# Performance work log

Hardware: AMD Instinct MI355X
Metric: run time of the kernel (lower is better)

## Reference

```python
import jax, jax.numpy as jnp
import numpy as np

D_MODEL = 2048
NUM_HEADS = 16
D_K = D_MODEL // NUM_HEADS
ROPE_THETA = 10000.0
B, S = 2, 2048


def setup_inputs() -> dict:
    key = jax.random.key(0)
    ks = jax.random.split(key, 5)
    std = 1.0 / np.sqrt(D_MODEL)
    return {
        "x": jax.random.normal(ks[0], (B, S, D_MODEL), jnp.float32),
        "wq": jax.random.normal(ks[1], (D_MODEL, D_MODEL), jnp.float32) * std,
        "wk": jax.random.normal(ks[2], (D_MODEL, D_MODEL), jnp.float32) * std,
        "wv": jax.random.normal(ks[3], (D_MODEL, D_MODEL), jnp.float32) * std,
        "wo": jax.random.normal(ks[4], (D_MODEL, D_MODEL), jnp.float32) * std,
        "token_positions": jnp.arange(S, dtype=jnp.int32),
    }


def _rope(x, positions):
    # x: [b, h, s, d_k]; positions: [s]
    inv_freq = 1.0 / (ROPE_THETA ** (jnp.arange(0, D_K, 2, dtype=jnp.float32) / D_K))
    freqs = positions.astype(jnp.float32)[:, None] * inv_freq[None, :]  # [s, d_k/2]
    cos, sin = jnp.cos(freqs), jnp.sin(freqs)
    x_even, x_odd = x[..., ::2], x[..., 1::2]
    out_even = x_even * cos - x_odd * sin
    out_odd = x_even * sin + x_odd * cos
    # re-interleave even/odd lanes
    return jnp.stack([out_even, out_odd], axis=-1).reshape(x.shape)


def reference(x, wq, wk, wv, wo, token_positions):
    b, s, _ = x.shape
    # projections: weight is [out, in] as in torch Linear-style einsum
    q = jnp.einsum("bsd,ed->bse", x, wq)
    k = jnp.einsum("bsd,ed->bse", x, wk)
    v = jnp.einsum("bsd,ed->bse", x, wv)
    # split heads: b s (h d) -> b h s d
    def split(t):
        return t.reshape(b, s, NUM_HEADS, D_K).transpose(0, 2, 1, 3)
    q, k, v = split(q), split(k), split(v)
    q = _rope(q, token_positions)
    k = _rope(k, token_positions)
    scores = jnp.einsum("bhmd,bhnd->bhmn", q, k) / jnp.sqrt(jnp.float32(D_K))
    causal = jnp.tril(jnp.ones((s, s), dtype=bool))
    scores = jnp.where(causal[None, None], scores, -jnp.inf)
    attn = jax.nn.softmax(scores, axis=-1)
    out = jnp.einsum("bhmn,bhnd->bhmd", attn, v)
    out = out.transpose(0, 2, 1, 3).reshape(b, s, D_MODEL)
    return jnp.einsum("em,bsm->bse", wo, out)
```

## Files before the change

### kernel.cpp

```cpp
#include <hip/hip_runtime.h>

#define S_LEN 2048
#define DM 2048
#define NH 16
#define DK 128
#define BB 2
#define BH (BB*NH)
#define GK 2048

typedef float f32x4 __attribute__((ext_vector_type(4)));
typedef float f32x16 __attribute__((ext_vector_type(16)));
typedef __bf16 bf16x8 __attribute__((ext_vector_type(8)));
typedef __bf16 bf16x2 __attribute__((ext_vector_type(2)));
typedef unsigned int u32;

#define AS1 __attribute__((address_space(1)))
#define AS3 __attribute__((address_space(3)))

__device__ inline void gload16(const void* g, void* l){
  __builtin_amdgcn_global_load_lds((AS1 const u32*)g, (AS3 u32*)l, 16, 0, 0);
}

__device__ inline ushort f2bf(float f){
  __bf16 h = (__bf16)f;
  ushort u;
  __builtin_memcpy(&u, &h, 2);
  return u;
}

__device__ inline u32 cvtpk(float a, float b){
  bf16x2 p; p[0] = (__bf16)a; p[1] = (__bf16)b;
  u32 r; __builtin_memcpy(&r, &p, 4); return r;
}

__global__ void k_f32_to_bf16(const float* __restrict__ in, ushort* __restrict__ out, int n4){
  int i = blockIdx.x * blockDim.x + threadIdx.x;
  if (i >= n4) return;
  float4 v = reinterpret_cast<const float4*>(in)[i];
  ushort4 o;
  o.x = f2bf(v.x); o.y = f2bf(v.y); o.z = f2bf(v.z); o.w = f2bf(v.w);
  reinterpret_cast<ushort4*>(out)[i] = o;
}

__global__ void k_w4(const float* __restrict__ wq, const float* __restrict__ wk,
                     const float* __restrict__ wv, const float* __restrict__ wo4,
                     ushort* __restrict__ dqkv, ushort* __restrict__ dwo){
  int i = blockIdx.x * 256 + threadIdx.x;
  int sel = i >> 20;
  int off = i & ((1 << 20) - 1);
  const float* s = (sel == 0) ? wq : (sel == 1) ? wk : (sel == 2) ? wv : wo4;
  ushort* d = (sel < 3) ? (dqkv + (size_t)sel * DM * DM) : dwo;
  float4 v = reinterpret_cast<const float4*>(s)[off];
  ushort4 o;
  o.x = f2bf(v.x); o.y = f2bf(v.y); o.z = f2bf(v.z); o.w = f2bf(v.w);
  reinterpret_cast<ushort4*>(d)[off] = o;
}

__global__ void k_rope_table(const int* __restrict__ pos, float2* __restrict__ cs){
  int idx = blockIdx.x * 256 + threadIdx.x;
  if (idx >= S_LEN * 64) return;
  int s = idx >> 6, i = idx & 63;
  float inv = expf(-0.14391156831212787f * (float)i);
  float f = (float)pos[s] * inv;
  cs[idx] = make_float2(cosf(f), sinf(f));
}

#define SBAR() do{ __builtin_amdgcn_s_barrier(); __builtin_amdgcn_sched_barrier(0); }while(0)
#define VMC(n) asm volatile("s_waitcnt vmcnt(" #n ")" ::: "memory")

#define STG(slot, srcp, tks, khh) do{ \
  const ushort* _s = (srcp) + (tks)*64 + (khh)*32; \
  gload16(_s,                    lds + (slot)*8192 + wid*512); \
  gload16(_s + (size_t)128*GK,   lds + (slot)*8192 + 4096 + wid*512); \
}while(0)

#define RD_A(slot, mh) do{ \
  af[0] = *reinterpret_cast<const bf16x8*>(ldsc + (slot)*16384 + wm*8192 + ((mh)*4+0)*1024 + frA); \
  af[1] = *reinterpret_cast<const bf16x8*>(ldsc + (slot)*16384 + wm*8192 + ((mh)*4+1)*1024 + frA); \
  af[2] = *reinterpret_cast<const bf16x8*>(ldsc + (slot)*16384 + wm*8192 + ((mh)*4+2)*1024 + frA); \
  af[3] = *reinterpret_cast<const bf16x8*>(ldsc + (slot)*16384 + wm*8192 + ((mh)*4+3)*1024 + frA); \
}while(0)

#define RD_B(slot) do{ \
  bfr[0] = *reinterpret_cast<const bf16x8*>(ldsc + (slot)*16384 + wn*4096 + 0*1024 + frA); \
  bfr[1] = *reinterpret_cast<const bf16x8*>(ldsc + (slot)*16384 + wn*4096 + 1*1024 + frA); \
  bfr[2] = *reinterpret_cast<const bf16x8*>(ldsc + (slot)*16384 + wn*4096 + 2*1024 + frA); \
  bfr[3] = *reinterpret_cast<const bf16x8*>(ldsc + (slot)*16384 + wn*4096 + 3*1024 + frA); \
}while(0)

#define MM(mh) do{ \
  __builtin_amdgcn_s_setprio(1); \
  _Pragma("unroll") \
  for (int mf2 = 0; mf2 < 4; mf2++) \
    _Pragma("unroll") \
    for (int nf = 0; nf < 4; nf++) \
      acc[(mh)*4+mf2][nf] = __builtin_amdgcn_mfma_f32_16x16x32_bf16(af[mf2], bfr[nf], acc[(mh)*4+mf2][nf], 0, 0, 0); \
  __builtin_amdgcn_s_setprio(0); \
}while(0)

__launch_bounds__(512, 2)
__global__ void k_gemm_qk(const ushort* __restrict__ A, const ushort* __restrict__ Bt,
                          const float2* __restrict__ cs,
                          ushort* __restrict__ Qh, ushort* __restrict__ Kh){
  __shared__ short lds[65536];
  const int tid = threadIdx.x, lane = tid & 63, wid = tid >> 6;
  const int wm = wid >> 2, wn = wid & 3;
  const int fr = lane & 15, fq = lane >> 4;

  const int bid = blockIdx.x;
  const int b2 = (bid & 7) * 32 + (bid >> 3);
  const int by = b2 >> 4, bx = b2 & 15;

  const int rbase = wid * 16 + (lane >> 2);
  const int kup = ((lane & 3) ^ ((lane >> 3) & 3)) * 8;
  const ushort* pa = A  + (size_t)(by * 256 + rbase) * GK + kup;
  const ushort* pb = Bt + (size_t)(bx * 256 + rbase) * GK + kup;

  const char* ldsc = (const char*)lds;
  const int frA = fr * 64 + ((fq * 16) ^ (((fr >> 1) & 3) << 4));

  f32x4 acc[8][4] = {};
  bf16x8 af[4], bfr[4];

  STG(0, pa, 0, 0); STG(1, pb, 0, 0); STG(2, pa, 0, 1); STG(3, pb, 0, 1);
  STG(4, pa, 1, 0); STG(5, pb, 1, 0);
  VMC(8);
  SBAR();

  #pragma unroll 1
  for (int it = 0; it < 16; ++it){
    const int tb  = 2 * it + 1;
    const int tn  = (2 * it + 2 < 32) ? 2 * it + 2 : 31;
    const int tn1 = (2 * it + 3 < 32) ? 2 * it + 3 : 31;
    RD_A(0, 0); RD_B(1); STG(6, pa, tb, 1);           SBAR(); MM(0); SBAR();
    RD_A(0, 1);          STG(7, pb, tb, 1);  VMC(6);  SBAR(); MM(1); SBAR();
    RD_A(2, 0); RD_B(3); STG(0, pa, tn, 0);           SBAR(); MM(0); SBAR();
    RD_A(2, 1);          STG(1, pb, tn, 0);  VMC(6);  SBAR(); MM(1); SBAR();
    RD_A(4, 0); RD_B(5); STG(2, pa, tn, 1);           SBAR(); MM(0); SBAR();
    RD_A(4, 1);          STG(3, pb, tn, 1);  VMC(6);  SBAR(); MM(1); SBAR();
    RD_A(6, 0); RD_B(7); STG(4, pa, tn1, 0);          SBAR(); MM(0); SBAR();
    RD_A(6, 1);          STG(5, pb, tn1, 0); VMC(6);  SBAR(); MM(1); SBAR();
  }

  const int rowb = by * 256 + wm * 128 + fq * 4;
  const bool isQ = (bx < 8);
  ushort* dst = isQ ? Qh : Kh;
  const float qscl = isQ ? 0.08838834764831845f : 1.0f;
  #pragma unroll
  for (int mf = 0; mf < 8; mf++)
    #pragma unroll
    for (int nf = 0; nf < 4; nf++){
      int col = bx * 256 + wn * 64 + nf * 16 + fr;
      int cg = col & 2047;
      int hh = cg >> 7, dd = cg & 127, jj = (cg >> 1) & 63;
      #pragma unroll
      for (int i = 0; i < 4; i++){
        int row = rowb + mf * 16 + i;
        int s = row & (S_LEN - 1), bb = row >> 11;
        float2 c2 = cs[s * 64 + jj];
        float v = acc[mf][nf][i];
        float p = __shfl_xor(v, 1);
        float o = (fr & 1) ? fmaf(p, c2.y, v * c2.x) : fmaf(v, c2.x, -p * c2.y);
        dst[((size_t)(bb * NH + hh) * S_LEN + s) * DK + dd] = f2bf(o * qscl);
      }
    }
}

#define WSTG_A(si, tks, khh) do{ \
  const ushort* _s = pa + (tks)*64 + (khh)*32; \
  gload16(_s,                  lds + (si)*8192 + wid*512); \
  gload16(_s + (size_t)128*GK, lds + (si)*8192 + 4096 + wid*512); \
}while(0)
#define WSTG_B(si, tks, khh) do{ \
  const ushort* _s = pb + (tks)*64 + (khh)*32; \
  gload16(_s, lds + 32768 + (si)*4096 + wid*512); \
}while(0)
#define WRD_A(si, mhf) do{ \
  af[0] = *reinterpret_cast<const bf16x8*>(ldsc + (si)*16384 + wm*4096 + ((mhf)*2+0)*1024 + frA); \
  af[1] = *reinterpret_cast<const bf16x8*>(ldsc + (si)*16384 + wm*4096 + ((mhf)*2+1)*1024 + frA); \
}while(0)
#define WRD_B(si) do{ \
  bfr[0] = *reinterpret_cast<const bf16x8*>(ldsc + 65536 + (si)*8192 + wn*4096 + 0*1024 + frA); \
  bfr[1] = *reinterpret_cast<const bf16x8*>(ldsc + 65536 + (si)*8192 + wn*4096 + 1*1024 + frA); \
  bfr[2] = *reinterpret_cast<const bf16x8*>(ldsc + 65536 + (si)*8192 + wn*4096 + 2*1024 + frA); \
  bfr[3] = *reinterpret_cast<const bf16x8*>(ldsc + 65536 + (si)*8192 + wn*4096 + 3*1024 + frA); \
}while(0)
#define WMM(mhf) do{ \
  __builtin_amdgcn_s_setprio(1); \
  _Pragma("unroll") \
  for (int k2 = 0; k2 < 2; k2++) \
    _Pragma("unroll") \
    for (int nf = 0; nf < 4; nf++) \
      acc[(mhf)*2+k2][nf] = __builtin_amdgcn_mfma_f32_16x16x32_bf16(af[k2], bfr[nf], acc[(mhf)*2+k2][nf], 0, 0, 0); \
  __builtin_amdgcn_s_setprio(0); \
}while(0)

#define WBODY() \
  WSTG_A(0, 0, 0); WSTG_B(0, 0, 0); WSTG_A(1, 0, 1); WSTG_B(1, 0, 1); \
  WSTG_A(2, 1, 0); WSTG_B(2, 1, 0); \
  VMC(6); \
  SBAR(); \
  _Pragma("unroll 1") \
  for (int it = 0; it < 16; ++it){ \
    const int tb  = 2 * it + 1; \
    const int tn  = (2 * it + 2 < 32) ? 2 * it + 2 : 31; \
    const int tn1 = (2 * it + 3 < 32) ? 2 * it + 3 : 31; \
    WRD_A(0, 0); WRD_B(0); WSTG_A(3, tb, 1);            SBAR(); WMM(0); SBAR(); \
    WRD_A(0, 1);           WSTG_B(3, tb, 1);  VMC(6);   SBAR(); WMM(1); SBAR(); \
    WRD_A(1, 0); WRD_B(1); WSTG_A(0, tn, 0);            SBAR(); WMM(0); SBAR(); \
    WRD_A(1, 1);           WSTG_B(0, tn, 0);  VMC(6);   SBAR(); WMM(1); SBAR(); \
    WRD_A(2, 0); WRD_B(2); WSTG_A(1, tn, 1);            SBAR(); WMM(0); SBAR(); \
    WRD_A(2, 1);           WSTG_B(1, tn, 1);  VMC(6);   SBAR(); WMM(1); SBAR(); \
    WRD_A(3, 0); WRD_B(3); WSTG_A(2, tn1, 0);           SBAR(); WMM(0); SBAR(); \
    WRD_A(3, 1);           WSTG_B(2, tn1, 0); VMC(6);   SBAR(); WMM(1); SBAR(); \
  }

__launch_bounds__(512, 2)
__global__ void k_gemm_v(const ushort* __restrict__ A, const ushort* __restrict__ Bt,
                         ushort* __restrict__ Vt){
  __shared__ short lds[49152];
  const int tid = threadIdx.x, lane = tid & 63, wid = tid >> 6;
  const int wm = wid >> 1, wn = wid & 1;
  const int fr = lane & 15, fq = lane >> 4;

  const int bid = blockIdx.x;
  const int b2 = (bid & 7) * 32 + (bid >> 3);
  const int by = b2 >> 4, bx = b2 & 15;

  const int rbase = wid * 16 + (lane >> 2);
  const int kup = ((lane & 3) ^ ((lane >> 3) & 3)) * 8;
  const ushort* pa = A  + (size_t)(by * 256 + rbase) * GK + kup;
  const ushort* pb = Bt + (size_t)(bx * 128 + rbase) * GK + kup;

  const char* ldsc = (const char*)lds;
  const int frA = fr * 64 + ((fq * 16) ^ (((fr >> 1) & 3) << 4));

  f32x4 acc[4][4] = {};
  bf16x8 af[2], bfr[4];

  WBODY();

  const int rowb = by * 256 + wm * 64 + fq * 4;
  #pragma unroll
  for (int mf = 0; mf < 4; mf++){
    int row0 = rowb + mf * 16;
    int s0 = row0 & (S_LEN - 1), bb = row0 >> 11;
    #pragma unroll
    for (int nf = 0; nf < 4; nf++){
      int col = bx * 128 + wn * 64 + nf * 16 + fr;
      int hh = col >> 7, dd = col & 127;
      ushort4 o;
      o.x = f2bf(acc[mf][nf][0]); o.y = f2bf(acc[mf][nf][1]);
      o.z = f2bf(acc[mf][nf][2]); o.w = f2bf(acc[mf][nf][3]);
      *reinterpret_cast<ushort4*>(&Vt[((size_t)(bb * NH + hh) * DK + dd) * S_LEN + s0]) = o;
    }
  }
}

__launch_bounds__(512, 2)
__global__ void k_gemm_wo(const ushort* __restrict__ A, const ushort* __restrict__ Bt,
                          float* __restrict__ C){
  __shared__ short lds[49152];
  const int tid = threadIdx.x, lane = tid & 63, wid = tid >> 6;
  const int wm = wid >> 1, wn = wid & 1;
  const int fr = lane & 15, fq = lane >> 4;

  const int bid = blockIdx.x;
  const int b2 = (bid & 7) * 32 + (bid >> 3);
  const int by = b2 >> 4, bx = b2 & 15;

  const int rbase = wid * 16 + (lane >> 2);
  const int kup = ((lane & 3) ^ ((lane >> 3) & 3)) * 8;
  const ushort* pa = A  + (size_t)(by * 256 + rbase) * GK + kup;
  const ushort* pb = Bt + (size_t)(bx * 128 + rbase) * GK + kup;

  const char* ldsc = (const char*)lds;
  const int frA = fr * 64 + ((fq * 16) ^ (((fr >> 1) & 3) << 4));

  f32x4 acc[4][4] = {};
  bf16x8 af[2], bfr[4];

  WBODY();

  const int orow = by * 256 + wm * 64 + fq * 4;
  const int ocol = bx * 128 + wn * 64 + fr;
  #pragma unroll
  for (int mf = 0; mf < 4; mf++)
    #pragma unroll
    for (int nf = 0; nf < 4; nf++)
      #pragma unroll
      for (int i = 0; i < 4; i++)
        C[(size_t)(orow + mf * 16 + i) * DM + ocol + nf * 16] = acc[mf][nf][i];
}

__launch_bounds__(256, 2)
__global__ void k_attn(const ushort* __restrict__ Q, const ushort* __restrict__ K,
                       const ushort* __restrict__ Vt, ushort* __restrict__ O){
  __shared__ short Kt[2][64 * 128];
  __shared__ short Vl[2][128 * 64];
  const int tid = threadIdx.x, lane = tid & 63, wid = tid >> 6;
  const int bid = blockIdx.x;
  const int bh = bid & 31, b = bh >> 4, hh = bh & 15;
  const int t8 = (bid >> 5) & 7;
  const int j = (bid < 256) ? (15 - t8) : t8;
  const int nt = 2 * j + 2;
  const int ql = lane & 31, h = lane >> 5;
  const int qrb = j * 128 + wid * 32;
  const int qrow = qrb + ql;
  const int swz = (ql & 7) << 4;

  const ushort* kbp = K  + (size_t)bh * S_LEN * DK;
  const ushort* vbp = Vt + (size_t)bh * DK * S_LEN;
  ushort* ob = O + (size_t)b * S_LEN * DM;

  int kro[4], kco[4], vro[4], vco[4];
  #pragma unroll
  for (int jj = 0; jj < 4; jj++){
    int ins = wid * 4 + jj;
    kro[jj] = ins * 4 + (lane >> 4);
    kco[jj] = 8 * ((lane & 15) ^ (kro[jj] & 7));
    vro[jj] = ins * 8 + (lane >> 3);
    vco[jj] = 8 * ((lane & 7) ^ (vro[jj] & 7));
  }

  bf16x8 qf[8];
  #pragma unroll
  for (int s = 0; s < 8; s++)
    qf[s] = *reinterpret_cast<const bf16x8*>(
        Q + ((size_t)bh * S_LEN + qrow) * DK + s * 16 + h * 8);

  float mi = -1e30f, li = 0.f;
  f32x16 accO[4] = {};

  #pragma unroll
  for (int jj = 0; jj < 4; jj++){
    int ins = wid * 4 + jj;
    gload16(kbp + (size_t)kro[jj] * DK + kco[jj],      (char*)Kt + ins * 1024);
    gload16(vbp + (size_t)vro[jj] * S_LEN + vco[jj],   (char*)Vl + ins * 1024);
  }
  __syncthreads();

  #pragma unroll 1
  for (int kt = 0; kt < nt; kt++){
    const int k0 = kt * 64;
    const int cur = kt & 1;
    if (kt + 1 < nt){
      const int k1 = k0 + 64;
      #pragma unroll
      for (int jj = 0; jj < 4; jj++){
        int ins = wid * 4 + jj;
        gload16(kbp + (size_t)(k1 + kro[jj]) * DK + kco[jj],  (char*)Kt + (cur ^ 1) * 16384 + ins * 1024);
        gload16(vbp + (size_t)vro[jj] * S_LEN + k1 + vco[jj], (char*)Vl + (cur ^ 1) * 16384 + ins * 1024);
      }
    }
    const char* KtB = (const char*)Kt + cur * 16384;
    const char* VlB = (const char*)Vl + cur * 16384;

    f32x16 sc[2] = {};
    #pragma unroll
    for (int s = 0; s < 8; s++){
      bf16x8 kf0 = *reinterpret_cast<const bf16x8*>(
          KtB + (ql) * 256 + ((s * 32 + h * 16) ^ swz));
      bf16x8 kf1 = *reinterpret_cast<const bf16x8*>(
          KtB + (32 + ql) * 256 + ((s * 32 + h * 16) ^ swz));
      sc[0] = __builtin_amdgcn_mfma_f32_32x32x16_bf16(kf0, qf[s], sc[0], 0, 0, 0);
      sc[1] = __builtin_amdgcn_mfma_f32_32x32x16_bf16(kf1, qf[s], sc[1], 0, 0, 0);
    }

    if (k0 + 63 > qrb){
      #pragma unroll
      for (int kb = 0; kb < 2; kb++)
        #pragma unroll
        for (int r = 0; r < 16; r++)
          if (k0 + kb * 32 + (r & 3) + 8 * (r >> 2) + 4 * h > qrow) sc[kb][r] = -1e30f;
    }

    float mx = sc[0][0];
    #pragma unroll
    for (int kb = 0; kb < 2; kb++)
      #pragma unroll
      for (int r = 0; r < 16; r++) mx = fmaxf(mx, sc[kb][r]);
    mx = fmaxf(mx, __shfl_xor(mx, 32));

    if (!__all(mx <= mi + 8.0f)){
      float mn = fmaxf(mi, mx);
      float scl = __expf(mi - mn);
      mi = mn;
      li *= scl;
      float sclr[16];
      #pragma unroll
      for (int r = 0; r < 16; r++) sclr[r] = __shfl(scl, (r & 3) + 8 * (r >> 2) + 4 * h);
      #pragma unroll
      for (int dt = 0; dt < 4; dt++)
        #pragma unroll
        for (int r = 0; r < 16; r++) accO[dt][r] *= sclr[r];
    }

    float rs = 0.f;
    #pragma unroll
    for (int kb = 0; kb < 2; kb++)
      #pragma unroll
      for (int r = 0; r < 16; r++){
        float e = __expf(sc[kb][r] - mi);
        sc[kb][r] = e;
        rs += e;
      }
    rs += __shfl_xor(rs, 32);
    li += rs;

    bf16x8 pf[4];
    #pragma unroll
    for (int t = 0; t < 4; t++){
      const int kbb = t >> 1, rb = (t & 1) * 8;
      u32 wA0 = cvtpk(sc[kbb][rb + 0], sc[kbb][rb + 1]);
      u32 wA1 = cvtpk(sc[kbb][rb + 2], sc[kbb][rb + 3]);
      u32 wB0 = cvtpk(sc[kbb][rb + 4], sc[kbb][rb + 5]);
      u32 wB1 = cvtpk(sc[kbb][rb + 6], sc[kbb][rb + 7]);
      u32 X = h ? wA0 : wB0;
      u32 Y = h ? wA1 : wB1;
      u32 x0 = (u32)__shfl_xor((int)X, 32);
      u32 x1 = (u32)__shfl_xor((int)Y, 32);
      u32 f[4];
      f[0] = h ? x0 : wA0;
      f[1] = h ? x1 : wA1;
      f[2] = h ? wB0 : x0;
      f[3] = h ? wB1 : x1;
      __builtin_memcpy(&pf[t], f, 16);
    }

    #pragma unroll
    for (int dt = 0; dt < 4; dt++){
      const int vrow = dt * 32 + ql;
      const int vswz = (vrow & 7) << 4;
      #pragma unroll
      for (int t = 0; t < 4; t++){
        bf16x8 vf = *reinterpret_cast<const bf16x8*>(
            VlB + vrow * 128 + ((t * 32 + h * 16) ^ vswz));
        accO[dt] = __builtin_amdgcn_mfma_f32_32x32x16_bf16(pf[t], vf, accO[dt], 0, 0, 0);
      }
    }
    __syncthreads();
  }

  float invr[16];
  #pragma unroll
  for (int r = 0; r < 16; r++) invr[r] = 1.f / __shfl(li, (r & 3) + 8 * (r >> 2) + 4 * h);
  #pragma unroll
  for (int dt = 0; dt < 4; dt++)
    #pragma unroll
    for (int r = 0; r < 16; r++){
      int row = qrb + (r & 3) + 8 * (r >> 2) + 4 * h;
      ob[(size_t)row * DM + hh * DK + dt * 32 + ql] = f2bf(accO[dt][r] * invr[r]);
    }
}

extern "C" void kernel_launch(void* const* d_in, const int* in_sizes, int n_in,
                              void* d_out, int out_size, void* d_ws, size_t ws_size,
                              hipStream_t stream){
  const float* x  = (const float*)d_in[0];
  const float* wq = (const float*)d_in[1];
  const float* wk = (const float*)d_in[2];
  const float* wv = (const float*)d_in[3];
  const float* wo = (const float*)d_in[4];
  const int* pos  = (const int*)d_in[5];
  float* out = (float*)d_out;

  char* ws = (char*)d_ws;
  ushort* xb   = (ushort*)(ws);
  ushort* Ob   = xb;
  ushort* wqkv = (ushort*)(ws + 16777216);
  ushort* Qh   = (ushort*)(ws + 41943040);
  ushort* Kh   = (ushort*)(ws + 58720256);
  ushort* Vt   = (ushort*)(ws + 75497472);
  float2* cs   = (float2*)(ws + 92274688);
  ushort* wob  = (ushort*)(ws + 93323264);

  const int M = BB * S_LEN;

  k_rope_table<<<(S_LEN * 64) / 256, 256, 0, stream>>>(pos, cs);
  k_f32_to_bf16<<<(M * DM / 4) / 256, 256, 0, stream>>>(x, xb, M * DM / 4);
  k_w4<<<4 * (DM * DM / 4) / 256, 256, 0, stream>>>(wq, wk, wv, wo, wqkv, wob);

  k_gemm_qk<<<256, 512, 0, stream>>>(xb, wqkv, cs, Qh, Kh);
  k_gemm_v<<<256, 512, 0, stream>>>(xb, wqkv + (size_t)2 * DM * DM, Vt);

  k_attn<<<512, 256, 0, stream>>>(Qh, Kh, Vt, Ob);

  k_gemm_wo<<<256, 512, 0, stream>>>(Ob, wob, out);
}
```

Before: 247.8 us.

## Software-pipeline attention QK with softmax/PV and merge conversion kernels

The attention main loop is restructured so each wave computes the QK^T scores for the next key tile while it does softmax and PV for the current tile. Two score register sets alternate, and the K and V loads are issued at separate points around the barriers. The goal is to overlap MFMA work with the exp/shuffle softmax work and with global-to-LDS loads. Separately, the x and weight fp32-to-bf16 conversion kernels are merged into one launch to save launch overhead. The extra score registers raise register pressure under the two-blocks-per-CU launch bound.

```diff
diff --git a/kernel.cpp b/kernel.cpp
--- a/kernel.cpp
+++ b/kernel.cpp
@@ -33,23 +33,20 @@
   u32 r; __builtin_memcpy(&r, &p, 4); return r;
 }
 
-__global__ void k_f32_to_bf16(const float* __restrict__ in, ushort* __restrict__ out, int n4){
-  int i = blockIdx.x * blockDim.x + threadIdx.x;
-  if (i >= n4) return;
-  float4 v = reinterpret_cast<const float4*>(in)[i];
-  ushort4 o;
-  o.x = f2bf(v.x); o.y = f2bf(v.y); o.z = f2bf(v.z); o.w = f2bf(v.w);
-  reinterpret_cast<ushort4*>(out)[i] = o;
-}
-
-__global__ void k_w4(const float* __restrict__ wq, const float* __restrict__ wk,
-                     const float* __restrict__ wv, const float* __restrict__ wo4,
-                     ushort* __restrict__ dqkv, ushort* __restrict__ dwo){
+__global__ void k_conv(const float* __restrict__ x, const float* __restrict__ wq,
+                       const float* __restrict__ wk, const float* __restrict__ wv,
+                       const float* __restrict__ wo4,
+                       ushort* __restrict__ xb, ushort* __restrict__ dqkv,
+                       ushort* __restrict__ dwo){
   int i = blockIdx.x * 256 + threadIdx.x;
   int sel = i >> 20;
   int off = i & ((1 << 20) - 1);
-  const float* s = (sel == 0) ? wq : (sel == 1) ? wk : (sel == 2) ? wv : wo4;
-  ushort* d = (sel < 3) ? (dqkv + (size_t)sel * DM * DM) : dwo;
+  const float* s; ushort* d;
+  if (sel < 2){ s = x + ((size_t)sel << 22); d = xb + ((size_t)sel << 22); }
+  else if (sel == 2){ s = wq; d = dqkv; }
+  else if (sel == 3){ s = wk; d = dqkv + (size_t)DM * DM; }
+  else if (sel == 4){ s = wv; d = dqkv + (size_t)2 * DM * DM; }
+  else { s = wo4; d = dwo; }
   float4 v = reinterpret_cast<const float4*>(s)[off];
   ushort4 o;
   o.x = f2bf(v.x); o.y = f2bf(v.y); o.z = f2bf(v.z); o.w = f2bf(v.w);
@@ -293,6 +290,78 @@
         C[(size_t)(orow + mf * 16 + i) * DM + ocol + nf * 16] = acc[mf][nf][i];
 }
 
+#define STK(tt) do{ char* _kd = (char*)Kt + ((tt) & 1) * 16384; \
+  _Pragma("unroll") for (int jj = 0; jj < 4; jj++){ \
+    int ins = wid * 4 + jj; \
+    gload16(kbp + (size_t)((tt) * 64 + kro[jj]) * DK + kco[jj], _kd + ins * 1024); } }while(0)
+
+#define STV(tt) do{ char* _vd = (char*)Vl + ((tt) & 1) * 16384; \
+  _Pragma("unroll") for (int jj = 0; jj < 4; jj++){ \
+    int ins = wid * 4 + jj; \
+    gload16(vbp + (size_t)vro[jj] * S_LEN + (tt) * 64 + vco[jj], _vd + ins * 1024); } }while(0)
+
+#define QKS(SC, tt) do{ \
+  const char* _KtB = (const char*)Kt + ((tt) & 1) * 16384; \
+  f32x16 _z = {}; SC[0] = _z; SC[1] = _z; \
+  _Pragma("unroll") for (int s = 0; s < 8; s++){ \
+    bf16x8 kf0 = *reinterpret_cast<const bf16x8*>(_KtB + ql * 256 + ((s*32 + h*16) ^ swz)); \
+    bf16x8 kf1 = *reinterpret_cast<const bf16x8*>(_KtB + (32 + ql) * 256 + ((s*32 + h*16) ^ swz)); \
+    SC[0] = __builtin_amdgcn_mfma_f32_32x32x16_bf16(kf0, qf[s], SC[0], 0, 0, 0); \
+    SC[1] = __builtin_amdgcn_mfma_f32_32x32x16_bf16(kf1, qf[s], SC[1], 0, 0, 0); \
+  } }while(0)
+
+#define SMPV(SC, tt) do{ \
+  const int _k0 = (tt) * 64; \
+  const char* _VlB = (const char*)Vl + ((tt) & 1) * 16384; \
+  if (_k0 + 63 > qrb){ \
+    _Pragma("unroll") for (int kb = 0; kb < 2; kb++) \
+      _Pragma("unroll") for (int r = 0; r < 16; r++) \
+        if (_k0 + kb * 32 + (r & 3) + 8 * (r >> 2) + 4 * h > qrow) SC[kb][r] = -1e30f; \
+  } \
+  float mx = SC[0][0]; \
+  _Pragma("unroll") for (int kb = 0; kb < 2; kb++) \
+    _Pragma("unroll") for (int r = 0; r < 16; r++) mx = fmaxf(mx, SC[kb][r]); \
+  mx = fmaxf(mx, __shfl_xor(mx, 32)); \
+  if (!__all(mx <= mi + 8.0f)){ \
+    float mn = fmaxf(mi, mx); \
+    float scl = __expf(mi - mn); \
+    mi = mn; li *= scl; \
+    float sclr[16]; \
+    _Pragma("unroll") for (int r = 0; r < 16; r++) sclr[r] = __shfl(scl, (r & 3) + 8 * (r >> 2) + 4 * h); \
+    _Pragma("unroll") for (int dt = 0; dt < 4; dt++) \
+      _Pragma("unroll") for (int r = 0; r < 16; r++) accO[dt][r] *= sclr[r]; \
+  } \
+  float rs = 0.f; \
+  _Pragma("unroll") for (int kb = 0; kb < 2; kb++) \
+    _Pragma("unroll") for (int r = 0; r < 16; r++){ \
+      float e = __expf(SC[kb][r] - mi); SC[kb][r] = e; rs += e; } \
+  rs += __shfl_xor(rs, 32); \
+  li += rs; \
+  bf16x8 pf[4]; \
+  _Pragma("unroll") for (int t2 = 0; t2 < 4; t2++){ \
+    const int kbb = t2 >> 1, rb = (t2 & 1) * 8; \
+    u32 wA0 = cvtpk(SC[kbb][rb + 0], SC[kbb][rb + 1]); \
+    u32 wA1 = cvtpk(SC[kbb][rb + 2], SC[kbb][rb + 3]); \
+    u32 wB0 = cvtpk(SC[kbb][rb + 4], SC[kbb][rb + 5]); \
+    u32 wB1 = cvtpk(SC[kbb][rb + 6], SC[kbb][rb + 7]); \
+    u32 X = h ? wA0 : wB0; \
+    u32 Y = h ? wA1 : wB1; \
+    u32 x0 = (u32)__shfl_xor((int)X, 32); \
+    u32 x1 = (u32)__shfl_xor((int)Y, 32); \
+    u32 fw[4]; \
+    fw[0] = h ? x0 : wA0; fw[1] = h ? x1 : wA1; \
+    fw[2] = h ? wB0 : x0; fw[3] = h ? wB1 : x1; \
+    __builtin_memcpy(&pf[t2], fw, 16); \
+  } \
+  _Pragma("unroll") for (int dt = 0; dt < 4; dt++){ \
+    const int vrow = dt * 32 + ql; \
+    const int vswz = (vrow & 7) << 4; \
+    _Pragma("unroll") for (int t2 = 0; t2 < 4; t2++){ \
+      bf16x8 vf = *reinterpret_cast<const bf16x8*>(_VlB + vrow * 128 + ((t2 * 32 + h * 16) ^ vswz)); \
+      accO[dt] = __builtin_amdgcn_mfma_f32_32x32x16_bf16(pf[t2], vf, accO[dt], 0, 0, 0); \
+    } \
+  } }while(0)
+
 __launch_bounds__(256, 2)
 __global__ void k_attn(const ushort* __restrict__ Q, const ushort* __restrict__ K,
                        const ushort* __restrict__ Vt, ushort* __restrict__ O){
@@ -331,116 +400,33 @@
 
   float mi = -1e30f, li = 0.f;
   f32x16 accO[4] = {};
-
-  #pragma unroll
-  for (int jj = 0; jj < 4; jj++){
-    int ins = wid * 4 + jj;
-    gload16(kbp + (size_t)kro[jj] * DK + kco[jj],      (char*)Kt + ins * 1024);
-    gload16(vbp + (size_t)vro[jj] * S_LEN + vco[jj],   (char*)Vl + ins * 1024);
+  f32x16 scA[2], scB[2];
+
+  STK(0); STV(0);
+  __syncthreads();
+  STK(1);
+  QKS(scA, 0);
+  __syncthreads();
+  STV(1);
+
+  int t = 1;
+  #pragma unroll 1
+  for (; t + 1 < nt; t += 2){
+    STK(t + 1);
+    QKS(scB, t);
+    SMPV(scA, t - 1);
+    __syncthreads();
+    STV(t + 1);
+    STK(t + 2);
+    QKS(scA, t + 1);
+    SMPV(scB, t);
+    __syncthreads();
+    STV(t + 2);
   }
+  QKS(scB, t);
+  SMPV(scA, t - 1);
   __syncthreads();
-
-  #pragma unroll 1
-  for (int kt = 0; kt < nt; kt++){
-    const int k0 = kt * 64;
-    const int cur = kt & 1;
-    if (kt + 1 < nt){
-      const int k1 = k0 + 64;
-      #pragma unroll
-      for (int jj = 0; jj < 4; jj++){
-        int ins = wid * 4 + jj;
-        gload16(kbp + (size_t)(k1 + kro[jj]) * DK + kco[jj],  (char*)Kt + (cur ^ 1) * 16384 + ins * 1024);
-        gload16(vbp + (size_t)vro[jj] * S_LEN + k1 + vco[jj], (char*)Vl + (cur ^ 1) * 16384 + ins * 1024);
-      }
-    }
-    const char* KtB = (const char*)Kt + cur * 16384;
-    const char* VlB = (const char*)Vl + cur * 16384;
-
-    f32x16 sc[2] = {};
-    #pragma unroll
-    for (int s = 0; s < 8; s++){
-      bf16x8 kf0 = *reinterpret_cast<const bf16x8*>(
-          KtB + (ql) * 256 + ((s * 32 + h * 16) ^ swz));
-      bf16x8 kf1 = *reinterpret_cast<const bf16x8*>(
-          KtB + (32 + ql) * 256 + ((s * 32 + h * 16) ^ swz));
-      sc[0] = __builtin_amdgcn_mfma_f32_32x32x16_bf16(kf0, qf[s], sc[0], 0, 0, 0);
-      sc[1] = __builtin_amdgcn_mfma_f32_32x32x16_bf16(kf1, qf[s], sc[1], 0, 0, 0);
-    }
-
-    if (k0 + 63 > qrb){
-      #pragma unroll
-      for (int kb = 0; kb < 2; kb++)
-        #pragma unroll
-        for (int r = 0; r < 16; r++)
-          if (k0 + kb * 32 + (r & 3) + 8 * (r >> 2) + 4 * h > qrow) sc[kb][r] = -1e30f;
-    }
-
-    float mx = sc[0][0];
-    #pragma unroll
-    for (int kb = 0; kb < 2; kb++)
-      #pragma unroll
-      for (int r = 0; r < 16; r++) mx = fmaxf(mx, sc[kb][r]);
-    mx = fmaxf(mx, __shfl_xor(mx, 32));
-
-    if (!__all(mx <= mi + 8.0f)){
-      float mn = fmaxf(mi, mx);
-      float scl = __expf(mi - mn);
-      mi = mn;
-      li *= scl;
-      float sclr[16];
-      #pragma unroll
-      for (int r = 0; r < 16; r++) sclr[r] = __shfl(scl, (r & 3) + 8 * (r >> 2) + 4 * h);
-      #pragma unroll
-      for (int dt = 0; dt < 4; dt++)
-        #pragma unroll
-        for (int r = 0; r < 16; r++) accO[dt][r] *= sclr[r];
-    }
-
-    float rs = 0.f;
-    #pragma unroll
-    for (int kb = 0; kb < 2; kb++)
-      #pragma unroll
-      for (int r = 0; r < 16; r++){
-        float e = __expf(sc[kb][r] - mi);
-        sc[kb][r] = e;
-        rs += e;
-      }
-    rs += __shfl_xor(rs, 32);
-    li += rs;
-
-    bf16x8 pf[4];
-    #pragma unroll
-    for (int t = 0; t < 4; t++){
-      const int kbb = t >> 1, rb = (t & 1) * 8;
-      u32 wA0 = cvtpk(sc[kbb][rb + 0], sc[kbb][rb + 1]);
-      u32 wA1 = cvtpk(sc[kbb][rb + 2], sc[kbb][rb + 3]);
-      u32 wB0 = cvtpk(sc[kbb][rb + 4], sc[kbb][rb + 5]);
-      u32 wB1 = cvtpk(sc[kbb][rb + 6], sc[kbb][rb + 7]);
-      u32 X = h ? wA0 : wB0;
-      u32 Y = h ? wA1 : wB1;
-      u32 x0 = (u32)__shfl_xor((int)X, 32);
-      u32 x1 = (u32)__shfl_xor((int)Y, 32);
-      u32 f[4];
-      f[0] = h ? x0 : wA0;
-      f[1] = h ? x1 : wA1;
-      f[2] = h ? wB0 : x0;
-      f[3] = h ? wB1 : x1;
-      __builtin_memcpy(&pf[t], f, 16);
-    }
-
-    #pragma unroll
-    for (int dt = 0; dt < 4; dt++){
-      const int vrow = dt * 32 + ql;
-      const int vswz = (vrow & 7) << 4;
-      #pragma unroll
-      for (int t = 0; t < 4; t++){
-        bf16x8 vf = *reinterpret_cast<const bf16x8*>(
-            VlB + vrow * 128 + ((t * 32 + h * 16) ^ vswz));
-        accO[dt] = __builtin_amdgcn_mfma_f32_32x32x16_bf16(pf[t], vf, accO[dt], 0, 0, 0);
-      }
-    }
-    __syncthreads();
-  }
+  SMPV(scB, t);
 
   float invr[16];
   #pragma unroll
@@ -475,11 +461,8 @@
   float2* cs   = (float2*)(ws + 92274688);
   ushort* wob  = (ushort*)(ws + 93323264);
 
-  const int M = BB * S_LEN;
-
   k_rope_table<<<(S_LEN * 64) / 256, 256, 0, stream>>>(pos, cs);
-  k_f32_to_bf16<<<(M * DM / 4) / 256, 256, 0, stream>>>(x, xb, M * DM / 4);
-  k_w4<<<4 * (DM * DM / 4) / 256, 256, 0, stream>>>(wq, wk, wv, wo, wqkv, wob);
+  k_conv<<<24576, 256, 0, stream>>>(x, wq, wk, wv, wo, xb, wqkv, wob);
 
   k_gemm_qk<<<256, 512, 0, stream>>>(xb, wqkv, cs, Qh, Kh);
   k_gemm_v<<<256, 512, 0, stream>>>(xb, wqkv + (size_t)2 * DM * DM, Vt);
```

Measured after the change: 245.3 us. No clear change (-1.0%).

## Merge conversion kernels and restructure attention into paired causal 64-row tiles

Applied to the files above, without the earlier changes.

Merges the rope-table, activation and weight bf16 conversion launches into one kernel to cut launch overhead. Reworks the attention kernel to 128-thread blocks, each handling two 64-row query tiles (j and 31-j) so causal work is balanced per block. It also drops the K/V double buffer for a single-buffered load with two barriers per tile, which loses load/compute overlap and halves waves per block.

```diff
diff --git a/kernel.cpp b/kernel.cpp
--- a/kernel.cpp
+++ b/kernel.cpp
@@ -33,36 +33,34 @@
   u32 r; __builtin_memcpy(&r, &p, 4); return r;
 }
 
-__global__ void k_f32_to_bf16(const float* __restrict__ in, ushort* __restrict__ out, int n4){
-  int i = blockIdx.x * blockDim.x + threadIdx.x;
-  if (i >= n4) return;
-  float4 v = reinterpret_cast<const float4*>(in)[i];
-  ushort4 o;
-  o.x = f2bf(v.x); o.y = f2bf(v.y); o.z = f2bf(v.z); o.w = f2bf(v.w);
-  reinterpret_cast<ushort4*>(out)[i] = o;
-}
-
-__global__ void k_w4(const float* __restrict__ wq, const float* __restrict__ wk,
-                     const float* __restrict__ wv, const float* __restrict__ wo4,
-                     ushort* __restrict__ dqkv, ushort* __restrict__ dwo){
-  int i = blockIdx.x * 256 + threadIdx.x;
+__global__ void k_conv(const float* __restrict__ x, const float* __restrict__ wq,
+                       const float* __restrict__ wk, const float* __restrict__ wv,
+                       const float* __restrict__ wo4,
+                       ushort* __restrict__ xb, ushort* __restrict__ dqkv,
+                       ushort* __restrict__ dwo,
+                       const int* __restrict__ pos, float2* __restrict__ cs){
+  int bid = blockIdx.x;
+  if (bid >= 24576){
+    int idx = (bid - 24576) * 256 + threadIdx.x;
+    int s = idx >> 6, i = idx & 63;
+    float inv = expf(-0.14391156831212787f * (float)i);
+    float f = (float)pos[s] * inv;
+    cs[idx] = make_float2(cosf(f), sinf(f));
+    return;
+  }
+  int i = bid * 256 + threadIdx.x;
   int sel = i >> 20;
   int off = i & ((1 << 20) - 1);
-  const float* s = (sel == 0) ? wq : (sel == 1) ? wk : (sel == 2) ? wv : wo4;
-  ushort* d = (sel < 3) ? (dqkv + (size_t)sel * DM * DM) : dwo;
+  const float* s; ushort* d;
+  if (sel < 2){ s = x + ((size_t)sel << 22); d = xb + ((size_t)sel << 22); }
+  else if (sel == 2){ s = wq; d = dqkv; }
+  else if (sel == 3){ s = wk; d = dqkv + (size_t)DM * DM; }
+  else if (sel == 4){ s = wv; d = dqkv + (size_t)2 * DM * DM; }
+  else { s = wo4; d = dwo; }
   float4 v = reinterpret_cast<const float4*>(s)[off];
   ushort4 o;
   o.x = f2bf(v.x); o.y = f2bf(v.y); o.z = f2bf(v.z); o.w = f2bf(v.w);
   reinterpret_cast<ushort4*>(d)[off] = o;
-}
-
-__global__ void k_rope_table(const int* __restrict__ pos, float2* __restrict__ cs){
-  int idx = blockIdx.x * 256 + threadIdx.x;
-  if (idx >= S_LEN * 64) return;
-  int s = idx >> 6, i = idx & 63;
-  float inv = expf(-0.14391156831212787f * (float)i);
-  float f = (float)pos[s] * inv;
-  cs[idx] = make_float2(cosf(f), sinf(f));
 }
 
 #define SBAR() do{ __builtin_amdgcn_s_barrier(); __builtin_amdgcn_sched_barrier(0); }while(0)
@@ -293,165 +291,158 @@
         C[(size_t)(orow + mf * 16 + i) * DM + ocol + nf * 16] = acc[mf][nf][i];
 }
 
-__launch_bounds__(256, 2)
+__launch_bounds__(128, 2)
 __global__ void k_attn(const ushort* __restrict__ Q, const ushort* __restrict__ K,
                        const ushort* __restrict__ Vt, ushort* __restrict__ O){
-  __shared__ short Kt[2][64 * 128];
-  __shared__ short Vl[2][128 * 64];
+  __shared__ short Kt[64 * 128];
+  __shared__ short Vl[128 * 64];
   const int tid = threadIdx.x, lane = tid & 63, wid = tid >> 6;
   const int bid = blockIdx.x;
-  const int bh = bid & 31, b = bh >> 4, hh = bh & 15;
-  const int t8 = (bid >> 5) & 7;
-  const int j = (bid < 256) ? (15 - t8) : t8;
-  const int nt = 2 * j + 2;
+  const int pid = bid >> 5;
+  const int bh = bid & 31;
+  const int b = bh >> 4, hh = bh & 15;
   const int ql = lane & 31, h = lane >> 5;
-  const int qrb = j * 128 + wid * 32;
-  const int qrow = qrb + ql;
   const int swz = (ql & 7) << 4;
 
   const ushort* kbp = K  + (size_t)bh * S_LEN * DK;
   const ushort* vbp = Vt + (size_t)bh * DK * S_LEN;
   ushort* ob = O + (size_t)b * S_LEN * DM;
 
-  int kro[4], kco[4], vro[4], vco[4];
+  int kro[8], kco[8], vro[8], vco[8];
   #pragma unroll
-  for (int jj = 0; jj < 4; jj++){
-    int ins = wid * 4 + jj;
+  for (int jj = 0; jj < 8; jj++){
+    int ins = wid * 8 + jj;
     kro[jj] = ins * 4 + (lane >> 4);
     kco[jj] = 8 * ((lane & 15) ^ (kro[jj] & 7));
     vro[jj] = ins * 8 + (lane >> 3);
     vco[jj] = 8 * ((lane & 7) ^ (vro[jj] & 7));
   }
 
-  bf16x8 qf[8];
-  #pragma unroll
-  for (int s = 0; s < 8; s++)
-    qf[s] = *reinterpret_cast<const bf16x8*>(
-        Q + ((size_t)bh * S_LEN + qrow) * DK + s * 16 + h * 8);
-
-  float mi = -1e30f, li = 0.f;
-  f32x16 accO[4] = {};
-
-  #pragma unroll
-  for (int jj = 0; jj < 4; jj++){
-    int ins = wid * 4 + jj;
-    gload16(kbp + (size_t)kro[jj] * DK + kco[jj],      (char*)Kt + ins * 1024);
-    gload16(vbp + (size_t)vro[jj] * S_LEN + vco[jj],   (char*)Vl + ins * 1024);
-  }
-  __syncthreads();
-
   #pragma unroll 1
-  for (int kt = 0; kt < nt; kt++){
-    const int k0 = kt * 64;
-    const int cur = kt & 1;
-    if (kt + 1 < nt){
-      const int k1 = k0 + 64;
-      #pragma unroll
-      for (int jj = 0; jj < 4; jj++){
-        int ins = wid * 4 + jj;
-        gload16(kbp + (size_t)(k1 + kro[jj]) * DK + kco[jj],  (char*)Kt + (cur ^ 1) * 16384 + ins * 1024);
-        gload16(vbp + (size_t)vro[jj] * S_LEN + k1 + vco[jj], (char*)Vl + (cur ^ 1) * 16384 + ins * 1024);
+  for (int half = 0; half < 2; half++){
+    const int j = half ? pid : 31 - pid;
+    const int qrb = j * 64 + wid * 32;
+    const int qrow = qrb + ql;
+    const int nt = j + 1;
+
+    bf16x8 qf[8];
+    #pragma unroll
+    for (int s = 0; s < 8; s++)
+      qf[s] = *reinterpret_cast<const bf16x8*>(
+          Q + ((size_t)bh * S_LEN + qrow) * DK + s * 16 + h * 8);
+
+    float mi = -1e30f, li = 0.f;
+    f32x16 accO[4] = {};
+
+    #pragma unroll 1
+    for (int kt = 0; kt < nt; kt++){
+      const int k0 = kt * 64;
+
+      __syncthreads();
+      #pragma unroll
+      for (int jj = 0; jj < 8; jj++){
+        int ins = wid * 8 + jj;
+        gload16(kbp + (size_t)(k0 + kro[jj]) * DK + kco[jj],  (char*)Kt + ins * 1024);
+        gload16(vbp + (size_t)vro[jj] * S_LEN + k0 + vco[jj], (char*)Vl + ins * 1024);
+      }
+      __syncthreads();
+
+      f32x16 sc[2] = {};
+      #pragma unroll
+      for (int s = 0; s < 8; s++){
+        bf16x8 kf0 = *reinterpret_cast<const bf16x8*>(
+            (const char*)Kt + ql * 256 + ((s * 32 + h * 16) ^ swz));
+        bf16x8 kf1 = *reinterpret_cast<const bf16x8*>(
+            (const char*)Kt + (32 + ql) * 256 + ((s * 32 + h * 16) ^ swz));
+        sc[0] = __builtin_amdgcn_mfma_f32_32x32x16_bf16(kf0, qf[s], sc[0], 0, 0, 0);
+        sc[1] = __builtin_amdgcn_mfma_f32_32x32x16_bf16(kf1, qf[s], sc[1], 0, 0, 0);
+      }
+
+      if (k0 + 63 > qrb){
+        #pragma unroll
+        for (int kb = 0; kb < 2; kb++)
+          #pragma unroll
+          for (int r = 0; r < 16; r++)
+            if (k0 + kb * 32 + (r & 3) + 8 * (r >> 2) + 4 * h > qrow) sc[kb][r] = -1e30f;
+      }
+
+      float mx = sc[0][0];
+      #pragma unroll
+      for (int kb = 0; kb < 2; kb++)
+        #pragma unroll
+        for (int r = 0; r < 16; r++) mx = fmaxf(mx, sc[kb][r]);
+      mx = fmaxf(mx, __shfl_xor(mx, 32));
+
+      if (!__all(mx <= mi + 8.0f)){
+        float mn = fmaxf(mi, mx);
+        float scl = __expf(mi - mn);
+        mi = mn;
+        li *= scl;
+        float sclr[16];
+        #pragma unroll
+        for (int r = 0; r < 16; r++) sclr[r] = __shfl(scl, (r & 3) + 8 * (r >> 2) + 4 * h);
+        #pragma unroll
+        for (int dt = 0; dt < 4; dt++)
+          #pragma unroll
+          for (int r = 0; r < 16; r++) accO[dt][r] *= sclr[r];
+      }
+
+      float rs = 0.f;
+      #pragma unroll
+      for (int kb = 0; kb < 2; kb++)
+        #pragma unroll
+        for (int r = 0; r < 16; r++){
+          float e = __expf(sc[kb][r] - mi);
+          sc[kb][r] = e;
+          rs += e;
+        }
+      rs += __shfl_xor(rs, 32);
+      li += rs;
+
+      bf16x8 pf[4];
+      #pragma unroll
+      for (int t = 0; t < 4; t++){
+        const int kbb = t >> 1, rb = (t & 1) * 8;
+        u32 wA0 = cvtpk(sc[kbb][rb + 0], sc[kbb][rb + 1]);
+        u32 wA1 = cvtpk(sc[kbb][rb + 2], sc[kbb][rb + 3]);
+        u32 wB0 = cvtpk(sc[kbb][rb + 4], sc[kbb][rb + 5]);
+        u32 wB1 = cvtpk(sc[kbb][rb + 6], sc[kbb][rb + 7]);
+        u32 X = h ? wA0 : wB0;
+        u32 Y = h ? wA1 : wB1;
+        u32 x0 = (u32)__shfl_xor((int)X, 32);
+        u32 x1 = (u32)__shfl_xor((int)Y, 32);
+        u32 f[4];
+        f[0] = h ? x0 : wA0;
+        f[1] = h ? x1 : wA1;
+        f[2] = h ? wB0 : x0;
+        f[3] = h ? wB1 : x1;
+        __builtin_memcpy(&pf[t], f, 16);
+      }
+
+      #pragma unroll
+      for (int dt = 0; dt < 4; dt++){
+        const int vrow = dt * 32 + ql;
+        const int vswz = (vrow & 7) << 4;
+        #pragma unroll
+        for (int t = 0; t < 4; t++){
+          bf16x8 vf = *reinterpret_cast<const bf16x8*>(
+              (const char*)Vl + vrow * 128 + ((t * 32 + h * 16) ^ vswz));
+          accO[dt] = __builtin_amdgcn_mfma_f32_32x32x16_bf16(pf[t], vf, accO[dt], 0, 0, 0);
+        }
       }
     }
-    const char* KtB = (const char*)Kt + cur * 16384;
-    const char* VlB = (const char*)Vl + cur * 16384;
-
-    f32x16 sc[2] = {};
-    #pragma unroll
-    for (int s = 0; s < 8; s++){
-      bf16x8 kf0 = *reinterpret_cast<const bf16x8*>(
-          KtB + (ql) * 256 + ((s * 32 + h * 16) ^ swz));
-      bf16x8 kf1 = *reinterpret_cast<const bf16x8*>(
-          KtB + (32 + ql) * 256 + ((s * 32 + h * 16) ^ swz));
-      sc[0] = __builtin_amdgcn_mfma_f32_32x32x16_bf16(kf0, qf[s], sc[0], 0, 0, 0);
-      sc[1] = __builtin_amdgcn_mfma_f32_32x32x16_bf16(kf1, qf[s], sc[1], 0, 0, 0);
-    }
-
-    if (k0 + 63 > qrb){
-      #pragma unroll
-      for (int kb = 0; kb < 2; kb++)
-        #pragma unroll
-        for (int r = 0; r < 16; r++)
-          if (k0 + kb * 32 + (r & 3) + 8 * (r >> 2) + 4 * h > qrow) sc[kb][r] = -1e30f;
-    }
-
-    float mx = sc[0][0];
-    #pragma unroll
-    for (int kb = 0; kb < 2; kb++)
-      #pragma unroll
-      for (int r = 0; r < 16; r++) mx = fmaxf(mx, sc[kb][r]);
-    mx = fmaxf(mx, __shfl_xor(mx, 32));
-
-    if (!__all(mx <= mi + 8.0f)){
-      float mn = fmaxf(mi, mx);
-      float scl = __expf(mi - mn);
-      mi = mn;
-      li *= scl;
-      float sclr[16];
-      #pragma unroll
-      for (int r = 0; r < 16; r++) sclr[r] = __shfl(scl, (r & 3) + 8 * (r >> 2) + 4 * h);
-      #pragma unroll
-      for (int dt = 0; dt < 4; dt++)
-        #pragma unroll
-        for (int r = 0; r < 16; r++) accO[dt][r] *= sclr[r];
-    }
-
-    float rs = 0.f;
-    #pragma unroll
-    for (int kb = 0; kb < 2; kb++)
+
+    float invr[16];
+    #pragma unroll
+    for (int r = 0; r < 16; r++) invr[r] = 1.f / __shfl(li, (r & 3) + 8 * (r >> 2) + 4 * h);
+    #pragma unroll
+    for (int dt = 0; dt < 4; dt++)
       #pragma unroll
       for (int r = 0; r < 16; r++){
-        float e = __expf(sc[kb][r] - mi);
-        sc[kb][r] = e;
-        rs += e;
-      }
-    rs += __shfl_xor(rs, 32);
-    li += rs;
-
-    bf16x8 pf[4];
-    #pragma unroll
-    for (int t = 0; t < 4; t++){
-      const int kbb = t >> 1, rb = (t & 1) * 8;
-      u32 wA0 = cvtpk(sc[kbb][rb + 0], sc[kbb][rb + 1]);
-      u32 wA1 = cvtpk(sc[kbb][rb + 2], sc[kbb][rb + 3]);
-      u32 wB0 = cvtpk(sc[kbb][rb + 4], sc[kbb][rb + 5]);
-      u32 wB1 = cvtpk(sc[kbb][rb + 6], sc[kbb][rb + 7]);
-      u32 X = h ? wA0 : wB0;
-      u32 Y = h ? wA1 : wB1;
-      u32 x0 = (u32)__shfl_xor((int)X, 32);
-      u32 x1 = (u32)__shfl_xor((int)Y, 32);
-      u32 f[4];
-      f[0] = h ? x0 : wA0;
-      f[1] = h ? x1 : wA1;
-      f[2] = h ? wB0 : x0;
-      f[3] = h ? wB1 : x1;
-      __builtin_memcpy(&pf[t], f, 16);
-    }
-
-    #pragma unroll
-    for (int dt = 0; dt < 4; dt++){
-      const int vrow = dt * 32 + ql;
-      const int vswz = (vrow & 7) << 4;
-      #pragma unroll
-      for (int t = 0; t < 4; t++){
-        bf16x8 vf = *reinterpret_cast<const bf16x8*>(
-            VlB + vrow * 128 + ((t * 32 + h * 16) ^ vswz));
-        accO[dt] = __builtin_amdgcn_mfma_f32_32x32x16_bf16(pf[t], vf, accO[dt], 0, 0, 0);
-      }
-    }
-    __syncthreads();
-  }
-
-  float invr[16];
-  #pragma unroll
-  for (int r = 0; r < 16; r++) invr[r] = 1.f / __shfl(li, (r & 3) + 8 * (r >> 2) + 4 * h);
-  #pragma unroll
-  for (int dt = 0; dt < 4; dt++)
-    #pragma unroll
-    for (int r = 0; r < 16; r++){
-      int row = qrb + (r & 3) + 8 * (r >> 2) + 4 * h;
-      ob[(size_t)row * DM + hh * DK + dt * 32 + ql] = f2bf(accO[dt][r] * invr[r]);
-    }
+        int row = qrb + (r & 3) + 8 * (r >> 2) + 4 * h;
+        ob[(size_t)row * DM + hh * DK + dt * 32 + ql] = f2bf(accO[dt][r] * invr[r]);
+      }
+  }
 }
 
 extern "C" void kernel_launch(void* const* d_in, const int* in_sizes, int n_in,
@@ -475,16 +466,12 @@
   float2* cs   = (float2*)(ws + 92274688);
   ushort* wob  = (ushort*)(ws + 93323264);
 
-  const int M = BB * S_LEN;
-
-  k_rope_table<<<(S_LEN * 64) / 256, 256, 0, stream>>>(pos, cs);
-  k_f32_to_bf16<<<(M * DM / 4) / 256, 256, 0, stream>>>(x, xb, M * DM / 4);
-  k_w4<<<4 * (DM * DM / 4) / 256, 256, 0, stream>>>(wq, wk, wv, wo, wqkv, wob);
+  k_conv<<<24576 + 512, 256, 0, stream>>>(x, wq, wk, wv, wo, xb, wqkv, wob, pos, cs);
 
   k_gemm_qk<<<256, 512, 0, stream>>>(xb, wqkv, cs, Qh, Kh);
   k_gemm_v<<<256, 512, 0, stream>>>(xb, wqkv + (size_t)2 * DM * DM, Vt);
 
-  k_attn<<<512, 256, 0, stream>>>(Qh, Kh, Vt, Ob);
+  k_attn<<<512, 128, 0, stream>>>(Qh, Kh, Vt, Ob);
 
   k_gemm_wo<<<256, 512, 0, stream>>>(Ob, wob, out);
 }
```

Result: no change. 251.0 us (+1.3%).
